# Performance work log

Hardware: AMD Instinct MI355X
Metric: run time of the kernel (lower is better)

The kernel has to match this reference:

```python
import jax, jax.numpy as jnp
import numpy as np

N_NODES = 100000
N_EDGES = 1600000
DIMS = [100, 200, 128, 128]
EPS = 1e-5


def setup_inputs() -> dict:
    key = jax.random.key(0)
    ks = jax.random.split(key, 32)
    inp = {
        "x": jax.random.normal(ks[0], (N_NODES, DIMS[0]), dtype=jnp.float32),
        "edge_row": jnp.sort(jax.random.randint(ks[1], (N_EDGES,), 0, N_NODES, dtype=jnp.int32)),
        "edge_col": jax.random.randint(ks[2], (N_EDGES,), 0, N_NODES, dtype=jnp.int32),
        "edge_val": jax.random.uniform(ks[3], (N_EDGES,), dtype=jnp.float32),
    }
    # GCwithself layer params: neighbor-agg linear W,b and self linear Ws,bs
    ki = 4
    for i in range(3):
        fi, fo = DIMS[i], DIMS[i + 1]
        s = 1.0 / np.sqrt(fi)
        inp[f"gc{i}_W"] = jax.random.uniform(ks[ki], (fi, fo), minval=-s, maxval=s); ki += 1
        inp[f"gc{i}_b"] = jnp.zeros((fo,), jnp.float32)
        inp[f"gc{i}_Ws"] = jax.random.uniform(ks[ki], (fi, fo), minval=-s, maxval=s); ki += 1
        inp[f"gc{i}_bs"] = jnp.zeros((fo,), jnp.float32)
    s = 1.0 / np.sqrt(128)
    inp["fc1_W"] = jax.random.uniform(ks[ki], (128, 128), minval=-s, maxval=s); ki += 1
    inp["fc1_b"] = jnp.zeros((128,), jnp.float32)
    inp["fc2a_W"] = jax.random.uniform(ks[ki], (128, 256), minval=-s, maxval=s); ki += 1
    inp["fc2a_b"] = jnp.zeros((256,), jnp.float32)
    inp["bn_g"] = jnp.ones((256,), jnp.float32)
    inp["bn_b"] = jnp.zeros((256,), jnp.float32)
    s2 = 1.0 / np.sqrt(256)
    inp["fc2b_W"] = jax.random.uniform(ks[ki], (256, 18), minval=-s2, maxval=s2); ki += 1
    inp["fc2b_b"] = jnp.zeros((18,), jnp.float32)
    return inp


def _gc_layer(x, row, col, val, W, b, Ws, bs):
    # spmm: (adj @ x) via gather + segment-sum, then linear + self-linear + ReLU
    agg = jax.ops.segment_sum(val[:, None] * x[col], row, num_segments=N_NODES)
    return jax.nn.relu(agg @ W + b + x @ Ws + bs)


def _batchnorm(h, g, b):
    mu = jnp.mean(h, axis=0)
    var = jnp.var(h, axis=0)
    return (h - mu) * jax.lax.rsqrt(var + EPS) * g + b


def reference(x, edge_row, edge_col, edge_val,
              gc0_W, gc0_b, gc0_Ws, gc0_bs,
              gc1_W, gc1_b, gc1_Ws, gc1_bs,
              gc2_W, gc2_b, gc2_Ws, gc2_bs,
              fc1_W, fc1_b, fc2a_W, fc2a_b, bn_g, bn_b, fc2b_W, fc2b_b):
    h = _gc_layer(x, edge_row, edge_col, edge_val, gc0_W, gc0_b, gc0_Ws, gc0_bs)
    h = _gc_layer(h, edge_row, edge_col, edge_val, gc1_W, gc1_b, gc1_Ws, gc1_bs)
    h = _gc_layer(h, edge_row, edge_col, edge_val, gc2_W, gc2_b, gc2_Ws, gc2_bs)
    h = jax.nn.relu(h @ fc1_W + fc1_b)
    h = _batchnorm(h @ fc2a_W + fc2a_b, bn_g, bn_b)
    h = jax.nn.relu(h)
    return h @ fc2b_W + fc2b_b
```

## Files before the change

### kernel.cpp

```cpp
#include <hip/hip_runtime.h>

#define N_NODES 100000
#define N_EDGES 1600000

#define MEMFENCE asm volatile("" ::: "memory")

typedef __attribute__((ext_vector_type(8))) short bf16x8;
typedef __attribute__((ext_vector_type(4))) float f32x4;

__device__ __forceinline__ unsigned short f2bf(float f) {
    unsigned u = __float_as_uint(f);
    u = (u + 0x7FFFu + ((u >> 16) & 1u)) >> 16;
    return (unsigned short)u;
}
__device__ __forceinline__ float bf2f(unsigned short h) {
    return __uint_as_float(((unsigned)h) << 16);
}
__device__ __forceinline__ float bflo(unsigned w) { return __uint_as_float(w << 16); }
__device__ __forceinline__ float bfhi(unsigned w) { return __uint_as_float(w & 0xFFFF0000u); }

__device__ __forceinline__ bf16x8 ld_frag(const unsigned short* p) {
    return *(const bf16x8*)p;
}

__global__ void build_row_ptr(const int* __restrict__ row, int* __restrict__ rp) {
    int n = blockIdx.x * blockDim.x + threadIdx.x;
    if (n > N_NODES) return;
    int lo = 0, hi = N_EDGES;
    while (lo < hi) {
        int mid = (lo + hi) >> 1;
        if (row[mid] < n) lo = mid + 1; else hi = mid;
    }
    rp[n] = lo;
}

__global__ __launch_bounds__(256) void conv_x(const float* __restrict__ x,
                                              unsigned short* __restrict__ xb) {
    const int total = N_NODES * 104;
    for (int i = blockIdx.x * 256 + threadIdx.x; i < total; i += gridDim.x * 256) {
        int r = i / 104, c = i - r * 104;
        xb[i] = (c < 100) ? f2bf(x[(size_t)r * 100 + c]) : (unsigned short)0;
    }
}

__global__ __launch_bounds__(256) void prep_all(
    const float* __restrict__ gc0W, const float* __restrict__ gc0Ws,
    const float* __restrict__ gc1W, const float* __restrict__ gc1Ws,
    const float* __restrict__ gc2W, const float* __restrict__ gc2Ws,
    const float* __restrict__ f1W,  const float* __restrict__ f2aW,
    const float* __restrict__ f2bW,
    const float* __restrict__ gc0b, const float* __restrict__ gc0bs,
    const float* __restrict__ gc2b, const float* __restrict__ gc2bs,
    const float* __restrict__ gc1b, const float* __restrict__ gc1bs,
    unsigned short* __restrict__ Bt0, unsigned short* __restrict__ Bt1,
    unsigned short* __restrict__ Bt2, unsigned short* __restrict__ Btf1,
    unsigned short* __restrict__ Btf2a, unsigned short* __restrict__ Btf2b,
    float* __restrict__ bias0, float* __restrict__ bias2, float* __restrict__ bias1)
{
    int i = blockIdx.x * 256 + threadIdx.x;
    if (i < 44800) {
        int n = i / 224, k = i - n * 224; float v = 0.f;
        if (k < 104) { if (k < 100) v = gc0W[(size_t)k * 200 + n]; }
        else { int kr = k - 104; if (kr < 100) v = gc0Ws[(size_t)kr * 200 + n]; }
        Bt0[i] = f2bf(v); return;
    }
    i -= 44800;
    if (i < 57344) {
        int n = i / 224, k = i - n * 224; float v = 0.f;
        if (k < 200) v = (n < 128) ? gc1W[(size_t)k * 128 + n] : gc1Ws[(size_t)k * 128 + (n - 128)];
        Bt1[i] = f2bf(v); return;
    }
    i -= 57344;
    if (i < 32768) {
        int n = i / 256, k = i - n * 256; float v;
        if (k < 128) v = gc2W[(size_t)k * 128 + n];
        else         v = gc2Ws[(size_t)(k - 128) * 128 + n];
        Bt2[i] = f2bf(v); return;
    }
    i -= 32768;
    if (i < 16384) { int n = i >> 7, k = i & 127; Btf1[i] = f2bf(f1W[(size_t)k * 128 + n]); return; }
    i -= 16384;
    if (i < 32768) { int n = i >> 7, k = i & 127; Btf2a[i] = f2bf(f2aW[(size_t)k * 256 + n]); return; }
    i -= 32768;
    if (i < 4608) { int n = i >> 8, k = i & 255; Btf2b[i] = f2bf(f2bW[(size_t)k * 18 + n]); return; }
    i -= 4608;
    if (i < 200) { bias0[i] = gc0b[i] + gc0bs[i]; return; }
    i -= 200;
    if (i < 128) { bias2[i] = gc2b[i] + gc2bs[i]; return; }
    i -= 128;
    if (i < 128) { bias1[i] = gc1b[i] + gc1bs[i]; return; }
}

template<int FUSE>
__global__ __launch_bounds__(256) void spmm_v5(
    const unsigned short* __restrict__ xin, int ldin, int F,
    const int* __restrict__ rp, const int* __restrict__ col,
    const float* __restrict__ val, const float* __restrict__ b01,
    unsigned short* __restrict__ outp, int ldout)
{
    const int node = blockIdx.x * 16 + (threadIdx.x >> 4);
    const int l16 = threadIdx.x & 15;
    const int f8 = l16 * 8;
    const bool act = f8 < F;
    const int e0 = rp[node], e1 = rp[node + 1];
    const unsigned short* xf = xin + f8;

    float a[8];
#pragma unroll
    for (int k = 0; k < 8; k++) a[k] = 0.f;

    for (int e = e0; e < e1; e += 8) {
        int   cj[8]; float vj[8];
#pragma unroll
        for (int j = 0; j < 8; j++) {
            int ej = e + j;
            bool m = ej < e1;
            int es = m ? ej : e0;
            cj[j] = col[es];
            float vv = val[es];
            vj[j] = m ? vv : 0.f;
        }
        if (act) {
            uint4 u[8];
#pragma unroll
            for (int j = 0; j < 8; j++)
                u[j] = *(const uint4*)(xf + (size_t)cj[j] * ldin);
#pragma unroll
            for (int j = 0; j < 8; j++) {
                float v = vj[j];
                a[0] += v * bflo(u[j].x); a[1] += v * bfhi(u[j].x);
                a[2] += v * bflo(u[j].y); a[3] += v * bfhi(u[j].y);
                a[4] += v * bflo(u[j].z); a[5] += v * bfhi(u[j].z);
                a[6] += v * bflo(u[j].w); a[7] += v * bfhi(u[j].w);
            }
        }
    }

    if (act) {
        if (FUSE) {
            uint4 uz = *(const uint4*)(xin + (size_t)node * ldin + 128 + f8);
            float z[8] = {bflo(uz.x), bfhi(uz.x), bflo(uz.y), bfhi(uz.y),
                          bflo(uz.z), bfhi(uz.z), bflo(uz.w), bfhi(uz.w)};
#pragma unroll
            for (int k = 0; k < 8; k++)
                a[k] = fmaxf(a[k] + z[k] + b01[f8 + k], 0.f);
        }
        uint4 pk;
        pk.x = ((unsigned)f2bf(a[1]) << 16) | (unsigned)f2bf(a[0]);
        pk.y = ((unsigned)f2bf(a[3]) << 16) | (unsigned)f2bf(a[2]);
        pk.z = ((unsigned)f2bf(a[5]) << 16) | (unsigned)f2bf(a[4]);
        pk.w = ((unsigned)f2bf(a[7]) << 16) | (unsigned)f2bf(a[6]);
        *(uint4*)(outp + (size_t)node * ldout + f8) = pk;
    }
}

__global__ __launch_bounds__(256) void gemm_head(
    const unsigned short* __restrict__ agg0, const unsigned short* __restrict__ xb,
    const unsigned short* __restrict__ Bt0, const float* __restrict__ bias0,
    const unsigned short* __restrict__ Bt1,
    unsigned short* __restrict__ yz, int M)
{
    __shared__ __align__(16) unsigned short H[64][264];

    const int tid = threadIdx.x;
    const int rowBase = blockIdx.x * 64;
    const int wave = tid >> 6, lane = tid & 63;
    const int cb = wave * 64;
    const int lrow = lane & 15, lq = lane >> 4;
    const int kq = lq * 8;

    {
        f32x4 acc[4][4] = {};
        {
            bf16x8 Bf[4][4];
#pragma unroll
            for (int ki = 0; ki < 4; ++ki)
#pragma unroll
                for (int n = 0; n < 4; ++n) {
                    int nr = cb + 16 * n + lrow;
                    bf16x8 t = {};
                    if (nr < 200) t = ld_frag(Bt0 + (size_t)nr * 224 + 32 * ki + kq);
                    Bf[ki][n] = t;
                }
            MEMFENCE;
            bf16x8 A2[2][4];
#pragma unroll
            for (int m = 0; m < 4; ++m) {
                int gr = rowBase + 16 * m + lrow;
                bf16x8 t = {};
                if (gr < M)
                    t = (kq < 104) ? ld_frag(agg0 + (size_t)gr * 104 + kq)
                                   : ld_frag(xb   + (size_t)gr * 104 + (kq - 104));
                A2[0][m] = t;
            }
            MEMFENCE;
#pragma unroll
            for (int ki = 0; ki < 4; ++ki) {
                const int cur = ki & 1;
                if (ki < 3) {
                    int k0 = 32 * (ki + 1) + kq;
#pragma unroll
                    for (int m = 0; m < 4; ++m) {
                        int gr = rowBase + 16 * m + lrow;
                        bf16x8 t = {};
                        if (gr < M)
                            t = (k0 < 104) ? ld_frag(agg0 + (size_t)gr * 104 + k0)
                                           : ld_frag(xb   + (size_t)gr * 104 + (k0 - 104));
                        A2[cur ^ 1][m] = t;
                    }
                }
                MEMFENCE;
#pragma unroll
                for (int m = 0; m < 4; ++m)
#pragma unroll
                    for (int n = 0; n < 4; ++n)
                        acc[m][n] = __builtin_amdgcn_mfma_f32_16x16x32_bf16(A2[cur][m], Bf[ki][n], acc[m][n], 0, 0, 0);
            }
        }
        {
            bf16x8 Bf[3][4];
#pragma unroll
            for (int ki = 0; ki < 3; ++ki)
#pragma unroll
                for (int n = 0; n < 4; ++n) {
                    int nr = cb + 16 * n + lrow;
                    bf16x8 t = {};
                    if (nr < 200) t = ld_frag(Bt0 + (size_t)nr * 224 + 32 * (ki + 4) + kq);
                    Bf[ki][n] = t;
                }
            MEMFENCE;
            bf16x8 A2[2][4];
#pragma unroll
            for (int m = 0; m < 4; ++m) {
                int gr = rowBase + 16 * m + lrow;
                int k0 = 128 + kq;
                bf16x8 t = {};
                if (gr < M && k0 < 208)
                    t = ld_frag(xb + (size_t)gr * 104 + (k0 - 104));
                A2[0][m] = t;
            }
            MEMFENCE;
#pragma unroll
            for (int ki = 0; ki < 3; ++ki) {
                const int cur = ki & 1;
                if (ki < 2) {
                    int k0 = 32 * (ki + 5) + kq;
#pragma unroll
                    for (int m = 0; m < 4; ++m) {
                        int gr = rowBase + 16 * m + lrow;
                        bf16x8 t = {};
                        if (gr < M && k0 < 208)
                            t = ld_frag(xb + (size_t)gr * 104 + (k0 - 104));
                        A2[cur ^ 1][m] = t;
                    }
                }
                MEMFENCE;
#pragma unroll
                for (int m = 0; m < 4; ++m)
#pragma unroll
                    for (int n = 0; n < 4; ++n)
                        acc[m][n] = __builtin_amdgcn_mfma_f32_16x16x32_bf16(A2[cur][m], Bf[ki][n], acc[m][n], 0, 0, 0);
            }
        }
#pragma unroll
        for (int n = 0; n < 4; ++n) {
            int colg = cb + 16 * n + lrow;
            if (colg >= 224) continue;
            float bb = (colg < 200) ? bias0[colg] : 0.f;
#pragma unroll
            for (int m = 0; m < 4; ++m)
#pragma unroll
                for (int r = 0; r < 4; ++r) {
                    int rowl = 16 * m + lq * 4 + r;
                    H[rowl][colg] = f2bf(fmaxf(acc[m][n][r] + bb, 0.f));
                }
        }
    }
    __syncthreads();

    {
        f32x4 acc[4][4] = {};
        {
            bf16x8 Bf[4][4];
#pragma unroll
            for (int ki = 0; ki < 4; ++ki)
#pragma unroll
                for (int n = 0; n < 4; ++n)
                    Bf[ki][n] = ld_frag(Bt1 + (size_t)(cb + 16 * n + lrow) * 224 + 32 * ki + kq);
            MEMFENCE;
#pragma unroll
            for (int ki = 0; ki < 4; ++ki) {
                bf16x8 af[4];
#pragma unroll
                for (int m = 0; m < 4; ++m) af[m] = *(const bf16x8*)&H[16 * m + lrow][32 * ki + kq];
#pragma unroll
                for (int m = 0; m < 4; ++m)
#pragma unroll
                    for (int n = 0; n < 4; ++n)
                        acc[m][n] = __builtin_amdgcn_mfma_f32_16x16x32_bf16(af[m], Bf[ki][n], acc[m][n], 0, 0, 0);
            }
        }
        {
            bf16x8 Bf[3][4];
#pragma unroll
            for (int ki = 0; ki < 3; ++ki)
#pragma unroll
                for (int n = 0; n < 4; ++n)
                    Bf[ki][n] = ld_frag(Bt1 + (size_t)(cb + 16 * n + lrow) * 224 + 32 * (ki + 4) + kq);
            MEMFENCE;
#pragma unroll
            for (int ki = 0; ki < 3; ++ki) {
                bf16x8 af[4];
#pragma unroll
                for (int m = 0; m < 4; ++m) af[m] = *(const bf16x8*)&H[16 * m + lrow][32 * (ki + 4) + kq];
#pragma unroll
                for (int m = 0; m < 4; ++m)
#pragma unroll
                    for (int n = 0; n < 4; ++n)
                        acc[m][n] = __builtin_amdgcn_mfma_f32_16x16x32_bf16(af[m], Bf[ki][n], acc[m][n], 0, 0, 0);
            }
        }
        __syncthreads();
#pragma unroll
        for (int n = 0; n < 4; ++n) {
            int colg = cb + 16 * n + lrow;
#pragma unroll
            for (int m = 0; m < 4; ++m)
#pragma unroll
                for (int r = 0; r < 4; ++r) {
                    int rowl = 16 * m + lq * 4 + r;
                    H[rowl][colg] = f2bf(acc[m][n][r]);
                }
        }
    }
    __syncthreads();
#pragma unroll
    for (int i = 0; i < 8; ++i) {
        int c = tid + 256 * i;
        int row = c >> 5;
        int ch  = c & 31;
        int rowg = rowBase + row;
        if (rowg < M)
            *(uint4*)(yz + (size_t)rowg * 256 + ch * 8) = *(const uint4*)&H[row][ch * 8];
    }
}

__global__ __launch_bounds__(256) void gemm_tail(
    const unsigned short* __restrict__ agg2, const unsigned short* __restrict__ h1,
    const unsigned short* __restrict__ Bt2, const float* __restrict__ bias2,
    const unsigned short* __restrict__ Btf1, const float* __restrict__ fc1b,
    const unsigned short* __restrict__ Btf2a, const float* __restrict__ fc2ab,
    unsigned short* __restrict__ h4, float* __restrict__ stats, int M)
{
    __shared__ __align__(16) unsigned short H[64][264];

    const int tid = threadIdx.x;
    const int rowBase = blockIdx.x * 64;
    const int wave = tid >> 6, lane = tid & 63;
    const int lrow = lane & 15, lq = lane >> 4;
    const int kq = lq * 8;

    {
        const int cb = wave * 32;
        f32x4 acc[4][2] = {};
        bf16x8 Bf[8][2];
#pragma unroll
        for (int ki = 0; ki < 8; ++ki)
#pragma unroll
            for (int n = 0; n < 2; ++n)
                Bf[ki][n] = ld_frag(Bt2 + (size_t)(cb + 16 * n + lrow) * 256 + 32 * ki + kq);
        MEMFENCE;
        bf16x8 A2[2][4];
#pragma unroll
        for (int m = 0; m < 4; ++m) {
            int gr = rowBase + 16 * m + lrow;
            bf16x8 t = {};
            if (gr < M) t = ld_frag(agg2 + (size_t)gr * 128 + kq);
            A2[0][m] = t;
        }
        MEMFENCE;
#pragma unroll
        for (int ki = 0; ki < 8; ++ki) {
            const int cur = ki & 1;
            if (ki < 7) {
                const int kin = ki + 1;
                int k0 = 32 * kin + kq;
                const unsigned short* Asrc = (kin < 4) ? agg2 : h1;
                int krel = (kin < 4) ? k0 : k0 - 128;
#pragma unroll
                for (int m = 0; m < 4; ++m) {
                    int gr = rowBase + 16 * m + lrow;
                    bf16x8 t = {};
                    if (gr < M) t = ld_frag(Asrc + (size_t)gr * 128 + krel);
                    A2[cur ^ 1][m] = t;
                }
            }
            MEMFENCE;
#pragma unroll
            for (int m = 0; m < 4; ++m)
#pragma unroll
                for (int n = 0; n < 2; ++n)
                    acc[m][n] = __builtin_amdgcn_mfma_f32_16x16x32_bf16(A2[cur][m], Bf[ki][n], acc[m][n], 0, 0, 0);
        }
#pragma unroll
        for (int n = 0; n < 2; ++n) {
            int colg = cb + 16 * n + lrow;
            float bb = bias2[colg];
#pragma unroll
            for (int m = 0; m < 4; ++m)
#pragma unroll
                for (int r = 0; r < 4; ++r) {
                    int rowl = 16 * m + lq * 4 + r;
                    H[rowl][colg] = f2bf(fmaxf(acc[m][n][r] + bb, 0.f));
                }
        }
    }
    __syncthreads();

    {
        const int cb = wave * 32;
        f32x4 acc[4][2] = {};
        bf16x8 Bf[4][2];
#pragma unroll
        for (int ki = 0; ki < 4; ++ki)
#pragma unroll
            for (int n = 0; n < 2; ++n)
                Bf[ki][n] = ld_frag(Btf1 + (size_t)(cb + 16 * n + lrow) * 128 + 32 * ki + kq);
        MEMFENCE;
#pragma unroll
        for (int ki = 0; ki < 4; ++ki) {
            bf16x8 af[4];
#pragma unroll
            for (int m = 0; m < 4; ++m) af[m] = *(const bf16x8*)&H[16 * m + lrow][32 * ki + kq];
#pragma unroll
            for (int m = 0; m < 4; ++m)
#pragma unroll
                for (int n = 0; n < 2; ++n)
                    acc[m][n] = __builtin_amdgcn_mfma_f32_16x16x32_bf16(af[m], Bf[ki][n], acc[m][n], 0, 0, 0);
        }
        __syncthreads();
#pragma unroll
        for (int n = 0; n < 2; ++n) {
            int colg = cb + 16 * n + lrow;
            float bb = fc1b[colg];
#pragma unroll
            for (int m = 0; m < 4; ++m)
#pragma unroll
                for (int r = 0; r < 4; ++r) {
                    int rowl = 16 * m + lq * 4 + r;
                    H[rowl][colg] = f2bf(fmaxf(acc[m][n][r] + bb, 0.f));
                }
        }
    }
    __syncthreads();

    {
        const int cb = wave * 64;
        f32x4 acc[4][4] = {};
        bf16x8 Bf[4][4];
#pragma unroll
        for (int ki = 0; ki < 4; ++ki)
#pragma unroll
            for (int n = 0; n < 4; ++n)
                Bf[ki][n] = ld_frag(Btf2a + (size_t)(cb + 16 * n + lrow) * 128 + 32 * ki + kq);
        MEMFENCE;
#pragma unroll
        for (int ki = 0; ki < 4; ++ki) {
            bf16x8 af[4];
#pragma unroll
            for (int m = 0; m < 4; ++m) af[m] = *(const bf16x8*)&H[16 * m + lrow][32 * ki + kq];
#pragma unroll
            for (int m = 0; m < 4; ++m)
#pragma unroll
                for (int n = 0; n < 4; ++n)
                    acc[m][n] = __builtin_amdgcn_mfma_f32_16x16x32_bf16(af[m], Bf[ki][n], acc[m][n], 0, 0, 0);
        }
        __syncthreads();

#pragma unroll
        for (int n = 0; n < 4; ++n) {
            int colg = cb + 16 * n + lrow;
            float bb = fc2ab[colg];
            float s = 0.f, s2 = 0.f;
#pragma unroll
            for (int m = 0; m < 4; ++m)
#pragma unroll
                for (int r = 0; r < 4; ++r) {
                    int rowl = 16 * m + lq * 4 + r;
                    float v = acc[m][n][r] + bb;
                    H[rowl][colg] = f2bf(v);
                    if (rowBase + rowl < M) { s += v; s2 += v * v; }
                }
            s  += __shfl_xor(s, 16);  s  += __shfl_xor(s, 32);
            s2 += __shfl_xor(s2, 16); s2 += __shfl_xor(s2, 32);
            if (lq == 0) {
                atomicAdd(&stats[colg], s);
                atomicAdd(&stats[256 + colg], s2);
            }
        }
        __syncthreads();
#pragma unroll
        for (int i = 0; i < 8; ++i) {
            int c = tid + 256 * i;
            int row = c >> 5;
            int ch  = c & 31;
            int rowg = rowBase + row;
            if (rowg < M)
                *(uint4*)(h4 + (size_t)rowg * 256 + ch * 8) = *(const uint4*)&H[row][ch * 8];
        }
    }
}

__global__ void bn_finalize(float* __restrict__ stats,
                            const float* __restrict__ g,
                            const float* __restrict__ b) {
    int t = threadIdx.x;
    const float invN = 1.f / (float)N_NODES;
    float mu = stats[t] * invN;
    float var = stats[256 + t] * invN - mu * mu;
    float sc = g[t] * rsqrtf(var + 1e-5f);
    stats[512 + t] = sc;
    stats[768 + t] = b[t] - mu * sc;
}

__global__ __launch_bounds__(256) void fc2b_kernel(
    const unsigned short* __restrict__ h4, const unsigned short* __restrict__ Btf2b,
    const float* __restrict__ bias, const float* __restrict__ stats,
    float* __restrict__ out, int M)
{
    const int tid = threadIdx.x;
    const int wave = tid >> 6, lane = tid & 63;
    const int lrow = lane & 15, lq = lane >> 4;
    const int kq = lq * 8;
    const int rowBase = blockIdx.x * 128 + wave * 32;

    f32x4 acc[2][2] = {};
    bf16x8 Bf[8][2];
#pragma unroll
    for (int ki = 0; ki < 8; ++ki)
#pragma unroll
        for (int n = 0; n < 2; ++n) {
            int nr = 16 * n + lrow;
            bf16x8 t = {};
            if (nr < 18) t = ld_frag(Btf2b + (size_t)nr * 256 + 32 * ki + kq);
            Bf[ki][n] = t;
        }
    MEMFENCE;
    uint4 ub[2][2];
#pragma unroll
    for (int m = 0; m < 2; ++m) {
        int gr = rowBase + 16 * m + lrow;
        uint4 u = make_uint4(0, 0, 0, 0);
        if (gr < M) u = *(const uint4*)(h4 + (size_t)gr * 256 + kq);
        ub[0][m] = u;
    }
    MEMFENCE;
#pragma unroll
    for (int ki = 0; ki < 8; ++ki) {
        const int cur = ki & 1;
        if (ki < 7) {
            int k0 = 32 * (ki + 1) + kq;
#pragma unroll
            for (int m = 0; m < 2; ++m) {
                int gr = rowBase + 16 * m + lrow;
                uint4 u = make_uint4(0, 0, 0, 0);
                if (gr < M) u = *(const uint4*)(h4 + (size_t)gr * 256 + k0);
                ub[cur ^ 1][m] = u;
            }
        }
        MEMFENCE;
        int k0 = 32 * ki + kq;
        const float* sc = stats + 512 + k0;
        const float* sh = stats + 768 + k0;
        bf16x8 af[2];
#pragma unroll
        for (int m = 0; m < 2; ++m) {
            unsigned w[4] = {ub[cur][m].x, ub[cur][m].y, ub[cur][m].z, ub[cur][m].w};
#pragma unroll
            for (int j = 0; j < 4; j++) {
                float lo = fmaxf(bflo(w[j]) * sc[2 * j] + sh[2 * j], 0.f);
                float hi = fmaxf(bfhi(w[j]) * sc[2 * j + 1] + sh[2 * j + 1], 0.f);
                w[j] = ((unsigned)f2bf(hi) << 16) | (unsigned)f2bf(lo);
            }
            uint4 packed = make_uint4(w[0], w[1], w[2], w[3]);
            af[m] = *(const bf16x8*)&packed;
        }
#pragma unroll
        for (int m = 0; m < 2; ++m)
#pragma unroll
            for (int n = 0; n < 2; ++n)
                acc[m][n] = __builtin_amdgcn_mfma_f32_16x16x32_bf16(af[m], Bf[ki][n], acc[m][n], 0, 0, 0);
    }
#pragma unroll
    for (int n = 0; n < 2; ++n) {
        int colg = 16 * n + lrow;
        if (colg >= 18) continue;
        float bb = bias[colg];
#pragma unroll
        for (int m = 0; m < 2; ++m)
#pragma unroll
            for (int r = 0; r < 4; ++r) {
                int rowg = rowBase + 16 * m + lq * 4 + r;
                if (rowg < M)
                    out[(size_t)rowg * 18 + colg] = acc[m][n][r] + bb;
            }
    }
}

extern "C" void kernel_launch(void* const* d_in, const int* in_sizes, int n_in,
                              void* d_out, int out_size, void* d_ws, size_t ws_size,
                              hipStream_t stream) {
    const float* x        = (const float*)d_in[0];
    const int*   edge_row = (const int*)  d_in[1];
    const int*   edge_col = (const int*)  d_in[2];
    const float* edge_val = (const float*)d_in[3];
    const float* gc0_W  = (const float*)d_in[4];
    const float* gc0_b  = (const float*)d_in[5];
    const float* gc0_Ws = (const float*)d_in[6];
    const float* gc0_bs = (const float*)d_in[7];
    const float* gc1_W  = (const float*)d_in[8];
    const float* gc1_b  = (const float*)d_in[9];
    const float* gc1_Ws = (const float*)d_in[10];
    const float* gc1_bs = (const float*)d_in[11];
    const float* gc2_W  = (const float*)d_in[12];
    const float* gc2_b  = (const float*)d_in[13];
    const float* gc2_Ws = (const float*)d_in[14];
    const float* gc2_bs = (const float*)d_in[15];
    const float* fc1_W  = (const float*)d_in[16];
    const float* fc1_b  = (const float*)d_in[17];
    const float* fc2a_W = (const float*)d_in[18];
    const float* fc2a_b = (const float*)d_in[19];
    const float* bn_g   = (const float*)d_in[20];
    const float* bn_b   = (const float*)d_in[21];
    const float* fc2b_W = (const float*)d_in[22];
    const float* fc2b_b = (const float*)d_in[23];
    float* out = (float*)d_out;

    char* ws = (char*)d_ws;
    int*   rowptr = (int*)ws;
    float* stats  = (float*)(ws + 512 * 1024);
    size_t o = 520 * 1024;
    unsigned short* Bt0   = (unsigned short*)(ws + o); o += 200 * 224 * 2;
    unsigned short* Bt1   = (unsigned short*)(ws + o); o += 256 * 224 * 2;
    unsigned short* Bt2   = (unsigned short*)(ws + o); o += 128 * 256 * 2;
    unsigned short* Btf1  = (unsigned short*)(ws + o); o += 128 * 128 * 2;
    unsigned short* Btf2a = (unsigned short*)(ws + o); o += 256 * 128 * 2;
    unsigned short* Btf2b = (unsigned short*)(ws + o); o += 18 * 256 * 2;
    float* bias0 = (float*)(ws + o); o += 200 * 4;
    float* bias2 = (float*)(ws + o); o += 128 * 4;
    float* bias1 = (float*)(ws + o); o += 128 * 4;
    const size_t SLOT = 52u * 1024 * 1024;
    char* S1 = ws + 1 * 1024 * 1024;
    char* S2 = S1 + SLOT;
    char* S3 = S2 + SLOT;

    unsigned short* xb   = (unsigned short*)S1;
    unsigned short* agg0 = (unsigned short*)S2;
    unsigned short* yz   = (unsigned short*)S3;
    unsigned short* h1   = (unsigned short*)S1;
    unsigned short* agg2 = (unsigned short*)S2;
    unsigned short* h4   = (unsigned short*)S3;

    build_row_ptr<<<392, 256, 0, stream>>>(edge_row, rowptr);
    conv_x<<<2048, 256, 0, stream>>>(x, xb);
    prep_all<<<(189128 + 255) / 256, 256, 0, stream>>>(
        gc0_W, gc0_Ws, gc1_W, gc1_Ws, gc2_W, gc2_Ws, fc1_W, fc2a_W, fc2b_W,
        gc0_b, gc0_bs, gc2_b, gc2_bs, gc1_b, gc1_bs,
        Bt0, Bt1, Bt2, Btf1, Btf2a, Btf2b, bias0, bias2, bias1);
    hipMemsetAsync(stats, 0, 512 * sizeof(float), stream);

    const int spmmGrid = N_NODES / 16;
    const int tile64 = (N_NODES + 63) / 64;

    spmm_v5<0><<<spmmGrid, 256, 0, stream>>>(xb, 104, 104, rowptr, edge_col, edge_val,
                                             nullptr, agg0, 104);
    gemm_head<<<tile64, 256, 0, stream>>>(agg0, xb, Bt0, bias0, Bt1, yz, N_NODES);
    spmm_v5<1><<<spmmGrid, 256, 0, stream>>>(yz, 256, 128, rowptr, edge_col, edge_val,
                                             bias1, h1, 128);
    spmm_v5<0><<<spmmGrid, 256, 0, stream>>>(h1, 128, 128, rowptr, edge_col, edge_val,
                                             nullptr, agg2, 128);
    gemm_tail<<<tile64, 256, 0, stream>>>(
        agg2, h1, Bt2, bias2, Btf1, fc1_b, Btf2a, fc2a_b, h4, stats, N_NODES);
    bn_finalize<<<1, 256, 0, stream>>>(stats, bn_g, bn_b);
    fc2b_kernel<<<(N_NODES + 127) / 128, 256, 0, stream>>>(
        h4, Btf2b, fc2b_b, stats, out, N_NODES);
}
```

Baseline: 525.0 us.

## Replace BN stat atomics with per-tile partials and shrink SpMM gather batch

Batchnorm statistics are now written by each gemm_tail block into a per-tile partial buffer, and a new 256-block reduction kernel sums them and computes scale/shift. This removes global float atomics and the memset. Separately, the SpMM inner loop now gathers 4 edges at a time instead of 8 with loads interleaved into the FMAs. That cuts register pressure but also leaves fewer loads in flight per thread. The partial buffer reuses an offset inside the agg2 slot, which relies on that region being unused by then.

```diff
diff --git a/kernel.cpp b/kernel.cpp
--- a/kernel.cpp
+++ b/kernel.cpp
@@ -2,6 +2,8 @@
 
 #define N_NODES 100000
 #define N_EDGES 1600000
+#define NTILE64 1563
+#define LDP 1568
 
 #define MEMFENCE asm volatile("" ::: "memory")
 
@@ -92,7 +94,7 @@
 }
 
 template<int FUSE>
-__global__ __launch_bounds__(256) void spmm_v5(
+__global__ __launch_bounds__(256) void spmm_v4(
     const unsigned short* __restrict__ xin, int ldin, int F,
     const int* __restrict__ rp, const int* __restrict__ col,
     const float* __restrict__ val, const float* __restrict__ b01,
@@ -109,10 +111,10 @@
 #pragma unroll
     for (int k = 0; k < 8; k++) a[k] = 0.f;
 
-    for (int e = e0; e < e1; e += 8) {
-        int   cj[8]; float vj[8];
-#pragma unroll
-        for (int j = 0; j < 8; j++) {
+    for (int e = e0; e < e1; e += 4) {
+        int   cj[4]; float vj[4];
+#pragma unroll
+        for (int j = 0; j < 4; j++) {
             int ej = e + j;
             bool m = ej < e1;
             int es = m ? ej : e0;
@@ -121,17 +123,14 @@
             vj[j] = m ? vv : 0.f;
         }
         if (act) {
-            uint4 u[8];
-#pragma unroll
-            for (int j = 0; j < 8; j++)
-                u[j] = *(const uint4*)(xf + (size_t)cj[j] * ldin);
-#pragma unroll
-            for (int j = 0; j < 8; j++) {
+#pragma unroll
+            for (int j = 0; j < 4; j++) {
+                uint4 u = *(const uint4*)(xf + (size_t)cj[j] * ldin);
                 float v = vj[j];
-                a[0] += v * bflo(u[j].x); a[1] += v * bfhi(u[j].x);
-                a[2] += v * bflo(u[j].y); a[3] += v * bfhi(u[j].y);
-                a[4] += v * bflo(u[j].z); a[5] += v * bfhi(u[j].z);
-                a[6] += v * bflo(u[j].w); a[7] += v * bfhi(u[j].w);
+                a[0] += v * bflo(u.x); a[1] += v * bfhi(u.x);
+                a[2] += v * bflo(u.y); a[3] += v * bfhi(u.y);
+                a[4] += v * bflo(u.z); a[5] += v * bfhi(u.z);
+                a[6] += v * bflo(u.w); a[7] += v * bfhi(u.w);
             }
         }
     }
@@ -350,7 +349,7 @@
     const unsigned short* __restrict__ Bt2, const float* __restrict__ bias2,
     const unsigned short* __restrict__ Btf1, const float* __restrict__ fc1b,
     const unsigned short* __restrict__ Btf2a, const float* __restrict__ fc2ab,
-    unsigned short* __restrict__ h4, float* __restrict__ stats, int M)
+    unsigned short* __restrict__ h4, float* __restrict__ P, int M)
 {
     __shared__ __align__(16) unsigned short H[64][264];
 
@@ -494,8 +493,8 @@
             s  += __shfl_xor(s, 16);  s  += __shfl_xor(s, 32);
             s2 += __shfl_xor(s2, 16); s2 += __shfl_xor(s2, 32);
             if (lq == 0) {
-                atomicAdd(&stats[colg], s);
-                atomicAdd(&stats[256 + colg], s2);
+                P[(size_t)colg * LDP + blockIdx.x] = s;
+                P[(size_t)(256 + colg) * LDP + blockIdx.x] = s2;
             }
         }
         __syncthreads();
@@ -511,16 +510,32 @@
     }
 }
 
-__global__ void bn_finalize(float* __restrict__ stats,
-                            const float* __restrict__ g,
-                            const float* __restrict__ b) {
-    int t = threadIdx.x;
-    const float invN = 1.f / (float)N_NODES;
-    float mu = stats[t] * invN;
-    float var = stats[256 + t] * invN - mu * mu;
-    float sc = g[t] * rsqrtf(var + 1e-5f);
-    stats[512 + t] = sc;
-    stats[768 + t] = b[t] - mu * sc;
+__global__ __launch_bounds__(256) void bn_reduce(const float* __restrict__ P,
+                                                 const float* __restrict__ g,
+                                                 const float* __restrict__ b,
+                                                 float* __restrict__ stats) {
+    const int c = blockIdx.x;
+    const int tid = threadIdx.x;
+    __shared__ float r1[256], r2[256];
+    float s = 0.f, s2 = 0.f;
+    for (int i = tid; i < NTILE64; i += 256) {
+        s  += P[(size_t)c * LDP + i];
+        s2 += P[(size_t)(256 + c) * LDP + i];
+    }
+    r1[tid] = s; r2[tid] = s2;
+    __syncthreads();
+    for (int off = 128; off > 0; off >>= 1) {
+        if (tid < off) { r1[tid] += r1[tid + off]; r2[tid] += r2[tid + off]; }
+        __syncthreads();
+    }
+    if (tid == 0) {
+        const float invN = 1.f / (float)N_NODES;
+        float mu = r1[0] * invN;
+        float var = r2[0] * invN - mu * mu;
+        float sc = g[c] * rsqrtf(var + 1e-5f);
+        stats[512 + c] = sc;
+        stats[768 + c] = b[c] - mu * sc;
+    }
 }
 
 __global__ __launch_bounds__(256) void fc2b_kernel(
@@ -660,6 +675,7 @@
     unsigned short* h1   = (unsigned short*)S1;
     unsigned short* agg2 = (unsigned short*)S2;
     unsigned short* h4   = (unsigned short*)S3;
+    float* Pp = (float*)(S2 + 40u * 1024 * 1024);
 
     build_row_ptr<<<392, 256, 0, stream>>>(edge_row, rowptr);
     conv_x<<<2048, 256, 0, stream>>>(x, xb);
@@ -667,21 +683,19 @@
         gc0_W, gc0_Ws, gc1_W, gc1_Ws, gc2_W, gc2_Ws, fc1_W, fc2a_W, fc2b_W,
         gc0_b, gc0_bs, gc2_b, gc2_bs, gc1_b, gc1_bs,
         Bt0, Bt1, Bt2, Btf1, Btf2a, Btf2b, bias0, bias2, bias1);
-    hipMemsetAsync(stats, 0, 512 * sizeof(float), stream);
 
     const int spmmGrid = N_NODES / 16;
-    const int tile64 = (N_NODES + 63) / 64;
-
-    spmm_v5<0><<<spmmGrid, 256, 0, stream>>>(xb, 104, 104, rowptr, edge_col, edge_val,
+
+    spmm_v4<0><<<spmmGrid, 256, 0, stream>>>(xb, 104, 104, rowptr, edge_col, edge_val,
                                              nullptr, agg0, 104);
-    gemm_head<<<tile64, 256, 0, stream>>>(agg0, xb, Bt0, bias0, Bt1, yz, N_NODES);
-    spmm_v5<1><<<spmmGrid, 256, 0, stream>>>(yz, 256, 128, rowptr, edge_col, edge_val,
+    gemm_head<<<NTILE64, 256, 0, stream>>>(agg0, xb, Bt0, bias0, Bt1, yz, N_NODES);
+    spmm_v4<1><<<spmmGrid, 256, 0, stream>>>(yz, 256, 128, rowptr, edge_col, edge_val,
                                              bias1, h1, 128);
-    spmm_v5<0><<<spmmGrid, 256, 0, stream>>>(h1, 128, 128, rowptr, edge_col, edge_val,
+    spmm_v4<0><<<spmmGrid, 256, 0, stream>>>(h1, 128, 128, rowptr, edge_col, edge_val,
                                              nullptr, agg2, 128);
-    gemm_tail<<<tile64, 256, 0, stream>>>(
-        agg2, h1, Bt2, bias2, Btf1, fc1_b, Btf2a, fc2a_b, h4, stats, N_NODES);
-    bn_finalize<<<1, 256, 0, stream>>>(stats, bn_g, bn_b);
+    gemm_tail<<<NTILE64, 256, 0, stream>>>(
+        agg2, h1, Bt2, bias2, Btf1, fc1_b, Btf2a, fc2a_b, h4, Pp, N_NODES);
+    bn_reduce<<<256, 256, 0, stream>>>(Pp, bn_g, bn_b, stats);
     fc2b_kernel<<<(N_NODES + 127) / 128, 256, 0, stream>>>(
         h4, Btf2b, fc2b_b, stats, out, N_NODES);
 }
```

Measured after the change: 508.4 us. 3.2% less time.
